# Kernel tuning notes

Measured on AMD Instinct MI355X. Metric: run time of the kernel, lower is better.

## Reference

```python
import jax, jax.numpy as jnp
import numpy as np

B, L, E, H, D = 2, 2048, 2048, 16, 128
EPS = 1e-6


def _rms(x, scale):
    # RMSNorm over head_dim, computed in float32 (matches torch RMSNorm)
    x32 = x.astype(jnp.float32)
    n = jnp.mean(x32 * x32, axis=-1, keepdims=True)
    return (scale.astype(jnp.float32) * (x32 * jax.lax.rsqrt(n + EPS))).astype(x.dtype)


def _rotary(x, rope):
    # x: [B, L, H, D]; rope: [B, L, D//2, 2]
    xs = x.astype(jnp.float32).reshape(*x.shape[:-1], -1, 2)  # [B,L,H,D/2,2]
    rc = rope.reshape(xs.shape[0], xs.shape[1], 1, xs.shape[3], 2).astype(jnp.float32)
    out = jnp.stack(
        [xs[..., 0] * rc[..., 0] - xs[..., 1] * rc[..., 1],
         xs[..., 1] * rc[..., 0] + xs[..., 0] * rc[..., 1]], -1)
    return out.reshape(x.shape).astype(x.dtype)


def setup_inputs() -> dict:
    key = jax.random.key(0)
    ks = jax.random.split(key, 9)
    s = 0.02  # weight init scale (~kaiming fan_in for E=2048)
    return {
        "inputs_q": jax.random.normal(ks[0], (B, L, E), jnp.float32),
        "inputs_kv": jax.random.normal(ks[1], (B, L, E), jnp.float32),
        "bias": jax.random.normal(ks[2], (B, 1, L, L), jnp.float32),
        "rope_q": jax.random.normal(ks[3], (B, L, D // 2, 2), jnp.float32),
        "rope_k": jax.random.normal(ks[4], (B, L, D // 2, 2), jnp.float32),
        "Wq": jax.random.normal(ks[5], (E, E), jnp.float32) * s,
        "Wk": jax.random.normal(ks[6], (E, E), jnp.float32) * s,
        "Wv": jax.random.normal(ks[7], (E, E), jnp.float32) * s,
        "Wo": jax.random.normal(ks[8], (E, E), jnp.float32) * s,
        "q_scale": jnp.ones((D,), jnp.float32),
        "k_scale": jnp.ones((D,), jnp.float32),
    }


def reference(inputs_q, inputs_kv, bias, rope_q, rope_k, Wq, Wk, Wv, Wo, q_scale, k_scale):
    Bq, Lq, _ = inputs_q.shape
    Lk = inputs_kv.shape[1]
    dtype = inputs_q.dtype
    # QKV projections (torch Linear: y = x @ W.T)
    q = (inputs_q @ Wq.T).reshape(Bq, Lq, H, D)
    k = (inputs_kv @ Wk.T).reshape(Bq, Lk, H, D)
    v = (inputs_kv @ Wv.T).reshape(Bq, Lk, H, D)
    # qk_norm
    q = _rms(q, q_scale)
    k = _rms(k, k_scale)
    # rotary embeddings
    q = _rotary(q, rope_q)
    k = _rotary(k, rope_k)
    # float32_logits
    q = q.astype(jnp.float32)
    k = k.astype(jnp.float32)
    # faithful to torch source: query.div_(depth ** (-0.5)) == q * sqrt(D)
    q = q / (D ** (-0.5))
    logits = jnp.einsum('bqhd,bkhd->bhqk', q, k) + bias.astype(jnp.float32)
    probs = jax.nn.softmax(logits, axis=-1).astype(dtype)
    # dropout_rate = 0.0 -> identity
    x = jnp.einsum('bhqk,bkhd->bqhd', probs, v).reshape(Bq, Lq, E)
    return x @ Wo.T
```

## Files before the change

### kernel.cpp

```cpp
#include <hip/hip_runtime.h>

#define Bb 2
#define Ll 2048
#define Ee 2048
#define Hh 16
#define Dd 128
#define BL (Bb * Ll)
#define NT (Ll / 64)
#define LOSCALE 1024.0f
#define INV_LOSCALE (1.0f / 1024.0f)

typedef float f32x4 __attribute__((ext_vector_type(4)));
typedef _Float16 f16x8 __attribute__((ext_vector_type(8)));

__device__ __forceinline__ void gld_lds16(const void* g, void* l) {
  __builtin_amdgcn_global_load_lds((const __attribute__((address_space(1))) void*)g,
                                   (__attribute__((address_space(3))) void*)l, 16, 0, 0);
}

__global__ __launch_bounds__(256) void cvt_f32_f16(const float* __restrict__ in,
                                                   _Float16* __restrict__ out, int n4) {
  int i = blockIdx.x * 256 + threadIdx.x;
  if (i < n4) {
    float4 f = ((const float4*)in)[i];
    _Float16 o[4] = {(_Float16)f.x, (_Float16)f.y, (_Float16)f.z, (_Float16)f.w};
    ((uint2*)out)[i] = *(uint2*)o;
  }
}

__global__ __launch_bounds__(256) void cvt_split(const float* __restrict__ in,
                                                 _Float16* __restrict__ hi,
                                                 _Float16* __restrict__ lo, int n4) {
  int i = blockIdx.x * 256 + threadIdx.x;
  if (i < n4) {
    float4 f = ((const float4*)in)[i];
    float fa[4] = {f.x, f.y, f.z, f.w};
    _Float16 h[4], l[4];
    for (int j = 0; j < 4; ++j) {
      h[j] = (_Float16)fa[j];
      l[j] = (_Float16)((fa[j] - (float)h[j]) * LOSCALE);
    }
    ((uint2*)hi)[i] = *(uint2*)h;
    ((uint2*)lo)[i] = *(uint2*)l;
  }
}

__global__ __launch_bounds__(256) void bias_perm(const float* __restrict__ bias,
                                                 _Float16* __restrict__ out) {
  __shared__ float T[128][68];
  const int kt = blockIdx.x, qt = blockIdx.y, b = blockIdx.z;
  const float* src = bias + ((size_t)b * Ll + qt * 128) * Ll + kt * 64;
  const int t = threadIdx.x;
  for (int c = 0; c < 8; ++c) {
    int idx = c * 256 + t;
    int r = idx >> 4, col4 = (idx & 15) * 4;
    float4 v = *(const float4*)&src[(size_t)r * Ll + col4];
    T[r][col4 + 0] = v.x; T[r][col4 + 1] = v.y;
    T[r][col4 + 2] = v.z; T[r][col4 + 3] = v.w;
  }
  __syncthreads();
  _Float16* dst = out + (((size_t)(b * 16 + qt) * NT + kt) * 8) * 64 * 16;
  for (int s = 0; s < 2; ++s) {
    int slot = t + s * 256;
    int w = slot >> 6, lane = slot & 63;
    int quad = lane >> 4, l16 = lane & 15;
    _Float16 vals[16];
    for (int nt = 0; nt < 4; ++nt)
      for (int r = 0; r < 4; ++r)
        vals[nt * 4 + r] = (_Float16)T[w * 16 + quad * 4 + r][nt * 16 + l16];
    *(uint4*)&dst[(size_t)slot * 16] = *(uint4*)&vals[0];
    *(uint4*)&dst[(size_t)slot * 16 + 8] = *(uint4*)&vals[8];
  }
}

template <typename OutT>
__global__ __launch_bounds__(256, 2) void gemm_bt(const _Float16* __restrict__ A,
                                                  const _Float16* __restrict__ Bw,
                                                  OutT* __restrict__ C, int M, int N, int K) {
  __shared__ _Float16 As[128 * 64];
  __shared__ _Float16 Bs[128 * 64];
  const int tid = threadIdx.x;
  const int wave = tid >> 6, lane = tid & 63;
  const int quad = lane >> 4, l16 = lane & 15;
  const int lrow = lane >> 3, lch = lane & 7;
  const int scol = (lch ^ lrow) * 8;
  const int bm = blockIdx.y * 128, bn = blockIdx.x * 128;
  const int wm = (wave >> 1) * 64, wn = (wave & 1) * 64;

  f32x4 acc[4][4] = {};

  for (int k0 = 0; k0 < K; k0 += 64) {
    for (int i = 0; i < 4; ++i) {
      int br = wave * 32 + i * 8;
      gld_lds16(&A[(size_t)(bm + br + lrow) * K + k0 + scol], &As[br * 64]);
      gld_lds16(&Bw[(size_t)(bn + br + lrow) * K + k0 + scol], &Bs[br * 64]);
    }
    __syncthreads();
    for (int ks = 0; ks < 2; ++ks) {
      f16x8 af[4], bf[4];
      for (int mt = 0; mt < 4; ++mt)
        af[mt] = *(const f16x8*)&As[(wm + mt * 16 + l16) * 64 +
                                    (((ks * 4 + quad) ^ (l16 & 7)) * 8)];
      for (int nt = 0; nt < 4; ++nt)
        bf[nt] = *(const f16x8*)&Bs[(wn + nt * 16 + l16) * 64 +
                                    (((ks * 4 + quad) ^ (l16 & 7)) * 8)];
      for (int mt = 0; mt < 4; ++mt)
        for (int nt = 0; nt < 4; ++nt)
          acc[mt][nt] = __builtin_amdgcn_mfma_f32_16x16x32_f16(af[mt], bf[nt], acc[mt][nt], 0, 0, 0);
    }
    __syncthreads();
  }

  for (int mt = 0; mt < 4; ++mt)
    for (int nt = 0; nt < 4; ++nt)
      for (int r = 0; r < 4; ++r) {
        int m = bm + wm + mt * 16 + quad * 4 + r;
        int n = bn + wn + nt * 16 + l16;
        C[(size_t)m * N + n] = (OutT)acc[mt][nt][r];
      }
}

__global__ __launch_bounds__(256, 2) void gemm_bt_split(
    const _Float16* __restrict__ Ah, const _Float16* __restrict__ Al,
    const _Float16* __restrict__ Bh, const _Float16* __restrict__ Bl,
    float* __restrict__ C, int M, int N, int K) {
  __shared__ _Float16 Ash[128 * 64];
  __shared__ _Float16 Asl[128 * 64];
  __shared__ _Float16 Bsh[128 * 64];
  __shared__ _Float16 Bsl[128 * 64];
  const int tid = threadIdx.x;
  const int wave = tid >> 6, lane = tid & 63;
  const int quad = lane >> 4, l16 = lane & 15;
  const int lrow = lane >> 3, lch = lane & 7;
  const int scol = (lch ^ lrow) * 8;
  const int bm = blockIdx.y * 128, bn = blockIdx.x * 128;
  const int wm = (wave >> 1) * 64, wn = (wave & 1) * 64;

  f32x4 acc_hh[4][4] = {};
  f32x4 acc_cr[4][4] = {};

  for (int k0 = 0; k0 < K; k0 += 64) {
    for (int i = 0; i < 4; ++i) {
      int br = wave * 32 + i * 8;
      size_t ga = (size_t)(bm + br + lrow) * K + k0 + scol;
      size_t gb = (size_t)(bn + br + lrow) * K + k0 + scol;
      gld_lds16(&Ah[ga], &Ash[br * 64]);
      gld_lds16(&Al[ga], &Asl[br * 64]);
      gld_lds16(&Bh[gb], &Bsh[br * 64]);
      gld_lds16(&Bl[gb], &Bsl[br * 64]);
    }
    __syncthreads();
    for (int ks = 0; ks < 2; ++ks) {
      const int sw = ((ks * 4 + quad) ^ (l16 & 7)) * 8;
      f16x8 afh[4], afl[4], bfh[4], bfl[4];
      for (int mt = 0; mt < 4; ++mt) {
        afh[mt] = *(const f16x8*)&Ash[(wm + mt * 16 + l16) * 64 + sw];
        afl[mt] = *(const f16x8*)&Asl[(wm + mt * 16 + l16) * 64 + sw];
      }
      for (int nt = 0; nt < 4; ++nt) {
        bfh[nt] = *(const f16x8*)&Bsh[(wn + nt * 16 + l16) * 64 + sw];
        bfl[nt] = *(const f16x8*)&Bsl[(wn + nt * 16 + l16) * 64 + sw];
      }
      for (int mt = 0; mt < 4; ++mt)
        for (int nt = 0; nt < 4; ++nt) {
          acc_hh[mt][nt] = __builtin_amdgcn_mfma_f32_16x16x32_f16(afh[mt], bfh[nt], acc_hh[mt][nt], 0, 0, 0);
          acc_cr[mt][nt] = __builtin_amdgcn_mfma_f32_16x16x32_f16(afh[mt], bfl[nt], acc_cr[mt][nt], 0, 0, 0);
          acc_cr[mt][nt] = __builtin_amdgcn_mfma_f32_16x16x32_f16(afl[mt], bfh[nt], acc_cr[mt][nt], 0, 0, 0);
        }
    }
    __syncthreads();
  }

  for (int mt = 0; mt < 4; ++mt)
    for (int nt = 0; nt < 4; ++nt)
      for (int r = 0; r < 4; ++r) {
        int m = bm + wm + mt * 16 + quad * 4 + r;
        int n = bn + wn + nt * 16 + l16;
        C[(size_t)m * N + n] = acc_hh[mt][nt][r] + acc_cr[mt][nt][r] * INV_LOSCALE;
      }
}

__global__ __launch_bounds__(256) void transpose_v(const _Float16* __restrict__ V,
                                                   _Float16* __restrict__ Vt) {
  __shared__ _Float16 T[64][72];
  const int bl0 = blockIdx.x * 64, n0 = blockIdx.y * 64;
  const int tid = threadIdx.x;
  for (int c = 0; c < 2; ++c) {
    int chunk = tid + c * 256;
    int r = chunk >> 3, cc = (chunk & 7) * 8;
    *(uint4*)&T[r][cc] = *(const uint4*)&V[(size_t)(bl0 + r) * Ee + n0 + cc];
  }
  __syncthreads();
  const int b = bl0 >> 11;
  const int k0 = bl0 & (Ll - 1);
  for (int c = 0; c < 2; ++c) {
    int chunk = tid + c * 256;
    int nr = chunk >> 3, kc = (chunk & 7) * 8;
    _Float16 tmp[8];
    for (int j = 0; j < 8; ++j) tmp[j] = T[kc + j][nr];
    *(uint4*)&Vt[((size_t)b * Ee + n0 + nr) * Ll + k0 + kc] = *(uint4*)tmp;
  }
}

__global__ __launch_bounds__(256) void rmsrope(const float* __restrict__ raw,
                                               const float* __restrict__ scale,
                                               const float* __restrict__ rope,
                                               _Float16* __restrict__ outh,
                                               _Float16* __restrict__ outl, float outmul) {
  int row = blockIdx.x * 4 + (threadIdx.x >> 6);
  int t = threadIdx.x & 63;
  float2 x = *(const float2*)&raw[(size_t)row * Dd + 2 * t];
  float ss = x.x * x.x + x.y * x.y;
  for (int off = 1; off < 64; off <<= 1) ss += __shfl_xor(ss, off);
  float inv = rsqrtf(ss * (1.0f / Dd) + 1e-6f);
  float2 sc = *(const float2*)&scale[2 * t];
  float y0 = x.x * inv * sc.x;
  float y1 = x.y * inv * sc.y;
  int bl = row >> 4;
  float2 cs = *(const float2*)&rope[(size_t)bl * Dd + 2 * t];
  float r0 = (y0 * cs.x - y1 * cs.y) * outmul;
  float r1 = (y1 * cs.x + y0 * cs.y) * outmul;
  _Float16 h[2] = {(_Float16)r0, (_Float16)r1};
  _Float16 l[2] = {(_Float16)((r0 - (float)h[0]) * LOSCALE),
                   (_Float16)((r1 - (float)h[1]) * LOSCALE)};
  *(uint*)&outh[(size_t)row * Dd + 2 * t] = *(uint*)h;
  *(uint*)&outl[(size_t)row * Dd + 2 * t] = *(uint*)l;
}

__global__ __launch_bounds__(512, 2) void attn(const _Float16* __restrict__ Qh_,
                                               const _Float16* __restrict__ Ql_,
                                               const _Float16* __restrict__ Kh_,
                                               const _Float16* __restrict__ Kl_,
                                               const _Float16* __restrict__ Vt_g,
                                               const _Float16* __restrict__ biasp,
                                               _Float16* __restrict__ O) {
  __shared__ _Float16 Ksh[2][64 * 128];
  __shared__ _Float16 Ksl[2][64 * 128];
  __shared__ _Float16 Vts[2][128 * 64];
  __shared__ _Float16 Ps[128 * 72];

  const int tid = threadIdx.x;
  const int wave = tid >> 6, lane = tid & 63;
  const int quad = lane >> 4, l16 = lane & 15;
  const int lrow8 = lane >> 3, lch8 = lane & 7;
  const int lrow16 = lane >> 4, lch16 = lane & 15;
  const int h = blockIdx.x;
  const int qt = blockIdx.y, q0 = qt * 128;
  const int b = blockIdx.z;

  f16x8 aqh[4], aql[4];
  {
    size_t qrow = (((size_t)b * Ll + q0 + wave * 16 + l16) * Hh + h) * Dd;
    for (int ks = 0; ks < 4; ++ks) {
      aqh[ks] = *(const f16x8*)&Qh_[qrow + ks * 32 + quad * 8];
      aql[ks] = *(const f16x8*)&Ql_[qrow + ks * 32 + quad * 8];
    }
  }
  const _Float16* Vbase = Vt_g + ((size_t)b * Ee + h * Dd) * Ll;
  const _Float16* bias_w =
      biasp + (((size_t)(b * 16 + qt) * NT * 8 + wave) * 64 + lane) * 16;

  f32x4 o_acc[8] = {};
  float m_r[4], l_r[4];
  for (int r = 0; r < 4; ++r) { m_r[r] = -1e30f; l_r[r] = 0.f; }

  auto stage = [&](int nb, int kt) {
    const int k0 = kt * 64;
    for (int i = 0; i < 2; ++i) {
      int br = wave * 8 + i * 4;
      int row = br + lrow16;
      int sc = (lch16 ^ (row & 7)) * 8;
      size_t g = (((size_t)b * Ll + k0 + row) * Hh + h) * Dd + sc;
      gld_lds16(&Kh_[g], &Ksh[nb][br * 128]);
      gld_lds16(&Kl_[g], &Ksl[nb][br * 128]);
    }
    for (int i = 0; i < 2; ++i) {
      int br = wave * 16 + i * 8;
      int row = br + lrow8;
      int sc = (lch8 ^ (row & 7)) * 8;
      gld_lds16(&Vbase[(size_t)row * Ll + k0 + sc], &Vts[nb][br * 64]);
    }
  };

  stage(0, 0);
  __syncthreads();

  for (int kt = 0; kt < NT; ++kt) {
    const int cur = kt & 1;
    if (kt + 1 < NT) stage(cur ^ 1, kt + 1);

    f16x8 bf0 = *(const f16x8*)&bias_w[(size_t)kt * 8192];
    f16x8 bf1 = *(const f16x8*)&bias_w[(size_t)kt * 8192 + 8];

    f32x4 s_hh[4] = {}, s_cr[4] = {};
    for (int ks = 0; ks < 4; ++ks) {
      const int sw = ((ks * 4 + quad) ^ (l16 & 7)) * 8;
      for (int nt = 0; nt < 4; ++nt) {
        f16x8 bkh = *(const f16x8*)&Ksh[cur][(nt * 16 + l16) * 128 + sw];
        f16x8 bkl = *(const f16x8*)&Ksl[cur][(nt * 16 + l16) * 128 + sw];
        s_hh[nt] = __builtin_amdgcn_mfma_f32_16x16x32_f16(aqh[ks], bkh, s_hh[nt], 0, 0, 0);
        s_cr[nt] = __builtin_amdgcn_mfma_f32_16x16x32_f16(aqh[ks], bkl, s_cr[nt], 0, 0, 0);
        s_cr[nt] = __builtin_amdgcn_mfma_f32_16x16x32_f16(aql[ks], bkh, s_cr[nt], 0, 0, 0);
      }
    }
#pragma unroll
    for (int nt = 0; nt < 4; ++nt)
#pragma unroll
      for (int r = 0; r < 4; ++r) {
        float bv = (nt < 2) ? (float)bf0[nt * 4 + r] : (float)bf1[nt * 4 + r - 8];
        s_hh[nt][r] += s_cr[nt][r] * INV_LOSCALE + bv;
      }

    float alpha[4];
    for (int r = 0; r < 4; ++r) {
      float x = fmaxf(fmaxf(s_hh[0][r], s_hh[1][r]), fmaxf(s_hh[2][r], s_hh[3][r]));
      for (int off = 1; off < 16; off <<= 1) x = fmaxf(x, __shfl_xor(x, off));
      float mn = fmaxf(m_r[r], x);
      alpha[r] = __expf(m_r[r] - mn);
      m_r[r] = mn;
    }
    for (int r = 0; r < 4; ++r) {
      float sum = 0.f;
      for (int nt = 0; nt < 4; ++nt) {
        float p = __expf(s_hh[nt][r] - m_r[r]);
        sum += p;
        Ps[(wave * 16 + quad * 4 + r) * 72 + nt * 16 + l16] = (_Float16)p;
      }
      for (int off = 1; off < 16; off <<= 1) sum += __shfl_xor(sum, off);
      l_r[r] = l_r[r] * alpha[r] + sum;
    }
    for (int ot = 0; ot < 8; ++ot)
      for (int r = 0; r < 4; ++r) o_acc[ot][r] *= alpha[r];

    for (int ks = 0; ks < 2; ++ks) {
      const int sw = ((ks * 4 + quad) ^ (l16 & 7)) * 8;
      f16x8 ap = *(const f16x8*)&Ps[(wave * 16 + l16) * 72 + ks * 32 + quad * 8];
      for (int ot = 0; ot < 8; ++ot) {
        f16x8 bv = *(const f16x8*)&Vts[cur][(ot * 16 + l16) * 64 + sw];
        o_acc[ot] = __builtin_amdgcn_mfma_f32_16x16x32_f16(ap, bv, o_acc[ot], 0, 0, 0);
      }
    }
    __syncthreads();
  }

  for (int ot = 0; ot < 8; ++ot)
    for (int r = 0; r < 4; ++r) {
      int m = q0 + wave * 16 + quad * 4 + r;
      O[(((size_t)b * Ll + m) * Hh + h) * Dd + ot * 16 + l16] =
          (_Float16)(o_acc[ot][r] / l_r[r]);
    }
}

extern "C" void kernel_launch(void* const* d_in, const int* in_sizes, int n_in,
                              void* d_out, int out_size, void* d_ws, size_t ws_size,
                              hipStream_t stream) {
  const float* inputs_q  = (const float*)d_in[0];
  const float* inputs_kv = (const float*)d_in[1];
  const float* bias      = (const float*)d_in[2];
  const float* rope_q    = (const float*)d_in[3];
  const float* rope_k    = (const float*)d_in[4];
  const float* Wq        = (const float*)d_in[5];
  const float* Wk        = (const float*)d_in[6];
  const float* Wv        = (const float*)d_in[7];
  const float* Wo        = (const float*)d_in[8];
  const float* q_scale   = (const float*)d_in[9];
  const float* k_scale   = (const float*)d_in[10];
  float* out = (float*)d_out;

  char* ws = (char*)d_ws;
  size_t o = 0;
  auto alloc = [&](size_t bytes) {
    char* p = ws + o;
    o += (bytes + 255) & ~(size_t)255;
    return p;
  };
  const size_t szX16 = (size_t)BL * Ee * 2;
  const size_t szW16 = (size_t)Ee * Ee * 2;
  _Float16* Xq_hi  = (_Float16*)alloc(szX16);
  _Float16* Xq_lo  = (_Float16*)alloc(szX16);
  _Float16* Xkv_hi = (_Float16*)alloc(szX16);
  _Float16* Xkv_lo = (_Float16*)alloc(szX16);
  _Float16* Wq_hi  = (_Float16*)alloc(szW16);
  _Float16* Wq_lo  = (_Float16*)alloc(szW16);
  _Float16* Wk_hi  = (_Float16*)alloc(szW16);
  _Float16* Wk_lo  = (_Float16*)alloc(szW16);
  _Float16* Wv_hi  = (_Float16*)alloc(szW16);
  _Float16* Wo_hi  = (_Float16*)alloc(szW16);
  float* Qraw = (float*)alloc((size_t)BL * Ee * 4);
  float* Kraw = (float*)alloc((size_t)BL * Ee * 4);
  _Float16* V16 = (_Float16*)alloc(szX16);
  _Float16* Q16h   = Xq_hi;
  _Float16* Q16l   = Xq_lo;
  _Float16* K16h   = Xkv_hi;
  _Float16* K16l   = Xkv_lo;
  _Float16* X16    = (_Float16*)Qraw;
  _Float16* Vt_g   = Wq_hi;
  _Float16* biasp  = (_Float16*)Kraw;

  const int nX4 = BL * Ee / 4;
  const int nW4 = Ee * Ee / 4;
  cvt_split<<<nX4 / 256, 256, 0, stream>>>(inputs_q, Xq_hi, Xq_lo, nX4);
  cvt_split<<<nX4 / 256, 256, 0, stream>>>(inputs_kv, Xkv_hi, Xkv_lo, nX4);
  cvt_split<<<nW4 / 256, 256, 0, stream>>>(Wq, Wq_hi, Wq_lo, nW4);
  cvt_split<<<nW4 / 256, 256, 0, stream>>>(Wk, Wk_hi, Wk_lo, nW4);
  cvt_f32_f16<<<nW4 / 256, 256, 0, stream>>>(Wv, Wv_hi, nW4);
  cvt_f32_f16<<<nW4 / 256, 256, 0, stream>>>(Wo, Wo_hi, nW4);

  dim3 gblk(Ee / 128, BL / 128);
  gemm_bt_split<<<gblk, 256, 0, stream>>>(Xq_hi, Xq_lo, Wq_hi, Wq_lo, Qraw, BL, Ee, Ee);
  gemm_bt_split<<<gblk, 256, 0, stream>>>(Xkv_hi, Xkv_lo, Wk_hi, Wk_lo, Kraw, BL, Ee, Ee);
  gemm_bt<_Float16><<<gblk, 256, 0, stream>>>(Xkv_hi, Wv_hi, V16, BL, Ee, Ee);

  transpose_v<<<dim3(BL / 64, Ee / 64), 256, 0, stream>>>(V16, Vt_g);

  rmsrope<<<BL * Hh / 4, 256, 0, stream>>>(Qraw, q_scale, rope_q, Q16h, Q16l, sqrtf((float)Dd));
  rmsrope<<<BL * Hh / 4, 256, 0, stream>>>(Kraw, k_scale, rope_k, K16h, K16l, 1.0f);

  bias_perm<<<dim3(NT, Ll / 128, Bb), 256, 0, stream>>>(bias, biasp);

  attn<<<dim3(Hh, Ll / 128, Bb), 512, 0, stream>>>(Q16h, Q16l, K16h, K16l, Vt_g, biasp, X16);

  gemm_bt<float><<<gblk, 256, 0, stream>>>(X16, Wo_hi, out, BL, Ee, Ee);
}
```

Baseline: 744.7 us.

## Double attention query tile per block, use exp2 softmax with lazy rescaling

The attention kernel now processes 256 query rows per block, with each wave handling two 16-row tiles. This halves K/V staging traffic per query and reuses each K/V LDS fragment across two MFMAs. The log2e factor is folded into the Q scaling and the bias so that softmax can use exp2. The running-max rescale is skipped unless the max grows by more than 8, and the row-sum shuffle reduction is deferred to the epilogue. The lo-part LOSCALE is removed so all three split MFMAs accumulate into one accumulator, and setprio hints plus an XOR-swizzled P buffer are added. The cost is doubled accumulator register pressure, and the unscaled fp16 lo parts may lose precision to subnormals.

```diff
diff --git a/kernel.cpp b/kernel.cpp
--- a/kernel.cpp
+++ b/kernel.cpp
@@ -9,6 +9,7 @@
 #define NT (Ll / 64)
 #define LOSCALE 1024.0f
 #define INV_LOSCALE (1.0f / 1024.0f)
+#define LOG2E 1.442695041f
 
 typedef float f32x4 __attribute__((ext_vector_type(4)));
 typedef _Float16 f16x8 __attribute__((ext_vector_type(8)));
@@ -59,7 +60,7 @@
     T[r][col4 + 2] = v.z; T[r][col4 + 3] = v.w;
   }
   __syncthreads();
-  _Float16* dst = out + (((size_t)(b * 16 + qt) * NT + kt) * 8) * 64 * 16;
+  _Float16* dst = out + ((((size_t)(b * 8 + (qt >> 1)) * NT + kt) * 16 + (qt & 1) * 8) * 64) * 16;
   for (int s = 0; s < 2; ++s) {
     int slot = t + s * 256;
     int w = slot >> 6, lane = slot & 63;
@@ -67,9 +68,9 @@
     _Float16 vals[16];
     for (int nt = 0; nt < 4; ++nt)
       for (int r = 0; r < 4; ++r)
-        vals[nt * 4 + r] = (_Float16)T[w * 16 + quad * 4 + r][nt * 16 + l16];
-    *(uint4*)&dst[(size_t)slot * 16] = *(uint4*)&vals[0];
-    *(uint4*)&dst[(size_t)slot * 16 + 8] = *(uint4*)&vals[8];
+        vals[nt * 4 + r] = (_Float16)(T[w * 16 + quad * 4 + r][nt * 16 + l16] * LOG2E);
+    *(uint4*)&dst[((size_t)w * 64 + lane) * 16] = *(uint4*)&vals[0];
+    *(uint4*)&dst[((size_t)w * 64 + lane) * 16 + 8] = *(uint4*)&vals[8];
   }
 }
 
@@ -221,8 +222,7 @@
   float r0 = (y0 * cs.x - y1 * cs.y) * outmul;
   float r1 = (y1 * cs.x + y0 * cs.y) * outmul;
   _Float16 h[2] = {(_Float16)r0, (_Float16)r1};
-  _Float16 l[2] = {(_Float16)((r0 - (float)h[0]) * LOSCALE),
-                   (_Float16)((r1 - (float)h[1]) * LOSCALE)};
+  _Float16 l[2] = {(_Float16)(r0 - (float)h[0]), (_Float16)(r1 - (float)h[1])};
   *(uint*)&outh[(size_t)row * Dd + 2 * t] = *(uint*)h;
   *(uint*)&outl[(size_t)row * Dd + 2 * t] = *(uint*)l;
 }
@@ -237,7 +237,7 @@
   __shared__ _Float16 Ksh[2][64 * 128];
   __shared__ _Float16 Ksl[2][64 * 128];
   __shared__ _Float16 Vts[2][128 * 64];
-  __shared__ _Float16 Ps[128 * 72];
+  __shared__ _Float16 Ps[256 * 64];
 
   const int tid = threadIdx.x;
   const int wave = tid >> 6, lane = tid & 63;
@@ -245,24 +245,25 @@
   const int lrow8 = lane >> 3, lch8 = lane & 7;
   const int lrow16 = lane >> 4, lch16 = lane & 15;
   const int h = blockIdx.x;
-  const int qt = blockIdx.y, q0 = qt * 128;
+  const int qt = blockIdx.y, q0 = qt * 256;
   const int b = blockIdx.z;
 
-  f16x8 aqh[4], aql[4];
-  {
-    size_t qrow = (((size_t)b * Ll + q0 + wave * 16 + l16) * Hh + h) * Dd;
+  f16x8 aqh[2][4], aql[2][4];
+  for (int m = 0; m < 2; ++m) {
+    size_t qrow = (((size_t)b * Ll + q0 + wave * 32 + m * 16 + l16) * Hh + h) * Dd;
     for (int ks = 0; ks < 4; ++ks) {
-      aqh[ks] = *(const f16x8*)&Qh_[qrow + ks * 32 + quad * 8];
-      aql[ks] = *(const f16x8*)&Ql_[qrow + ks * 32 + quad * 8];
+      aqh[m][ks] = *(const f16x8*)&Qh_[qrow + ks * 32 + quad * 8];
+      aql[m][ks] = *(const f16x8*)&Ql_[qrow + ks * 32 + quad * 8];
     }
   }
   const _Float16* Vbase = Vt_g + ((size_t)b * Ee + h * Dd) * Ll;
-  const _Float16* bias_w =
-      biasp + (((size_t)(b * 16 + qt) * NT * 8 + wave) * 64 + lane) * 16;
-
-  f32x4 o_acc[8] = {};
-  float m_r[4], l_r[4];
-  for (int r = 0; r < 4; ++r) { m_r[r] = -1e30f; l_r[r] = 0.f; }
+  const _Float16* bias_base = biasp + (size_t)(b * 8 + qt) * NT * 16 * 1024 +
+                              (size_t)(wave * 2) * 1024 + (size_t)lane * 16;
+
+  f32x4 o_acc[2][8] = {};
+  float m_r[2][4], l_r[2][4];
+  for (int m = 0; m < 2; ++m)
+    for (int r = 0; r < 4; ++r) { m_r[m][r] = -1e30f; l_r[m][r] = 0.f; }
 
   auto stage = [&](int nb, int kt) {
     const int k0 = kt * 64;
@@ -287,68 +288,106 @@
 
   for (int kt = 0; kt < NT; ++kt) {
     const int cur = kt & 1;
+
+    f16x8 bf[2][2];
+    for (int m = 0; m < 2; ++m) {
+      const _Float16* bp = bias_base + ((size_t)kt * 16 + m) * 1024;
+      bf[m][0] = *(const f16x8*)&bp[0];
+      bf[m][1] = *(const f16x8*)&bp[8];
+    }
     if (kt + 1 < NT) stage(cur ^ 1, kt + 1);
 
-    f16x8 bf0 = *(const f16x8*)&bias_w[(size_t)kt * 8192];
-    f16x8 bf1 = *(const f16x8*)&bias_w[(size_t)kt * 8192 + 8];
-
-    f32x4 s_hh[4] = {}, s_cr[4] = {};
+    __builtin_amdgcn_s_setprio(1);
+    f32x4 s[2][4] = {};
     for (int ks = 0; ks < 4; ++ks) {
       const int sw = ((ks * 4 + quad) ^ (l16 & 7)) * 8;
       for (int nt = 0; nt < 4; ++nt) {
         f16x8 bkh = *(const f16x8*)&Ksh[cur][(nt * 16 + l16) * 128 + sw];
         f16x8 bkl = *(const f16x8*)&Ksl[cur][(nt * 16 + l16) * 128 + sw];
-        s_hh[nt] = __builtin_amdgcn_mfma_f32_16x16x32_f16(aqh[ks], bkh, s_hh[nt], 0, 0, 0);
-        s_cr[nt] = __builtin_amdgcn_mfma_f32_16x16x32_f16(aqh[ks], bkl, s_cr[nt], 0, 0, 0);
-        s_cr[nt] = __builtin_amdgcn_mfma_f32_16x16x32_f16(aql[ks], bkh, s_cr[nt], 0, 0, 0);
-      }
-    }
+        for (int m = 0; m < 2; ++m) {
+          s[m][nt] = __builtin_amdgcn_mfma_f32_16x16x32_f16(aqh[m][ks], bkh, s[m][nt], 0, 0, 0);
+          s[m][nt] = __builtin_amdgcn_mfma_f32_16x16x32_f16(aql[m][ks], bkh, s[m][nt], 0, 0, 0);
+          s[m][nt] = __builtin_amdgcn_mfma_f32_16x16x32_f16(aqh[m][ks], bkl, s[m][nt], 0, 0, 0);
+        }
+      }
+    }
+    __builtin_amdgcn_s_setprio(0);
+
 #pragma unroll
-    for (int nt = 0; nt < 4; ++nt)
+    for (int m = 0; m < 2; ++m)
 #pragma unroll
+      for (int nt = 0; nt < 4; ++nt)
+#pragma unroll
+        for (int r = 0; r < 4; ++r) {
+          float bv = (nt < 2) ? (float)bf[m][0][nt * 4 + r] : (float)bf[m][1][nt * 4 + r - 8];
+          s[m][nt][r] += bv;
+        }
+
+    float x[2][4];
+    bool grow = false;
+    for (int m = 0; m < 2; ++m)
       for (int r = 0; r < 4; ++r) {
-        float bv = (nt < 2) ? (float)bf0[nt * 4 + r] : (float)bf1[nt * 4 + r - 8];
-        s_hh[nt][r] += s_cr[nt][r] * INV_LOSCALE + bv;
-      }
-
-    float alpha[4];
-    for (int r = 0; r < 4; ++r) {
-      float x = fmaxf(fmaxf(s_hh[0][r], s_hh[1][r]), fmaxf(s_hh[2][r], s_hh[3][r]));
-      for (int off = 1; off < 16; off <<= 1) x = fmaxf(x, __shfl_xor(x, off));
-      float mn = fmaxf(m_r[r], x);
-      alpha[r] = __expf(m_r[r] - mn);
-      m_r[r] = mn;
-    }
-    for (int r = 0; r < 4; ++r) {
-      float sum = 0.f;
-      for (int nt = 0; nt < 4; ++nt) {
-        float p = __expf(s_hh[nt][r] - m_r[r]);
-        sum += p;
-        Ps[(wave * 16 + quad * 4 + r) * 72 + nt * 16 + l16] = (_Float16)p;
-      }
-      for (int off = 1; off < 16; off <<= 1) sum += __shfl_xor(sum, off);
-      l_r[r] = l_r[r] * alpha[r] + sum;
-    }
-    for (int ot = 0; ot < 8; ++ot)
-      for (int r = 0; r < 4; ++r) o_acc[ot][r] *= alpha[r];
-
+        float v = fmaxf(fmaxf(s[m][0][r], s[m][1][r]), fmaxf(s[m][2][r], s[m][3][r]));
+        for (int off = 1; off < 16; off <<= 1) v = fmaxf(v, __shfl_xor(v, off));
+        x[m][r] = v;
+        grow |= (v > m_r[m][r] + 8.f);
+      }
+    if (__any(grow)) {
+      for (int m = 0; m < 2; ++m)
+        for (int r = 0; r < 4; ++r) {
+          float mn = fmaxf(m_r[m][r], x[m][r]);
+          float alpha = exp2f(m_r[m][r] - mn);
+          m_r[m][r] = mn;
+          l_r[m][r] *= alpha;
+          for (int ot = 0; ot < 8; ++ot) o_acc[m][ot][r] *= alpha;
+        }
+    }
+    for (int m = 0; m < 2; ++m)
+      for (int r = 0; r < 4; ++r) {
+        int row = wave * 32 + m * 16 + quad * 4 + r;
+        float sum = 0.f;
+        for (int nt = 0; nt < 4; ++nt) {
+          float p = exp2f(s[m][nt][r] - m_r[m][r]);
+          sum += p;
+          int col = nt * 16 + l16;
+          Ps[row * 64 + (col ^ (((row >> 2) & 3) << 4))] = (_Float16)p;
+        }
+        l_r[m][r] += sum;
+      }
+
+    __builtin_amdgcn_s_setprio(1);
     for (int ks = 0; ks < 2; ++ks) {
       const int sw = ((ks * 4 + quad) ^ (l16 & 7)) * 8;
-      f16x8 ap = *(const f16x8*)&Ps[(wave * 16 + l16) * 72 + ks * 32 + quad * 8];
+      f16x8 ap[2];
+      for (int m = 0; m < 2; ++m) {
+        int prow = wave * 32 + m * 16 + l16;
+        ap[m] = *(const f16x8*)&Ps[prow * 64 +
+                                   ((ks * 32 + quad * 8) ^ (((l16 >> 2) & 3) << 4))];
+      }
       for (int ot = 0; ot < 8; ++ot) {
         f16x8 bv = *(const f16x8*)&Vts[cur][(ot * 16 + l16) * 64 + sw];
-        o_acc[ot] = __builtin_amdgcn_mfma_f32_16x16x32_f16(ap, bv, o_acc[ot], 0, 0, 0);
-      }
-    }
+        for (int m = 0; m < 2; ++m)
+          o_acc[m][ot] = __builtin_amdgcn_mfma_f32_16x16x32_f16(ap[m], bv, o_acc[m][ot], 0, 0, 0);
+      }
+    }
+    __builtin_amdgcn_s_setprio(0);
     __syncthreads();
   }
 
-  for (int ot = 0; ot < 8; ++ot)
+  for (int m = 0; m < 2; ++m)
     for (int r = 0; r < 4; ++r) {
-      int m = q0 + wave * 16 + quad * 4 + r;
-      O[(((size_t)b * Ll + m) * Hh + h) * Dd + ot * 16 + l16] =
-          (_Float16)(o_acc[ot][r] / l_r[r]);
-    }
+      float l = l_r[m][r];
+      for (int off = 1; off < 16; off <<= 1) l += __shfl_xor(l, off);
+      l_r[m][r] = 1.f / l;
+    }
+
+  for (int m = 0; m < 2; ++m)
+    for (int ot = 0; ot < 8; ++ot)
+      for (int r = 0; r < 4; ++r) {
+        int mm = q0 + wave * 32 + m * 16 + quad * 4 + r;
+        O[(((size_t)b * Ll + mm) * Hh + h) * Dd + ot * 16 + l16] =
+            (_Float16)(o_acc[m][ot][r] * l_r[m][r]);
+      }
 }
 
 extern "C" void kernel_launch(void* const* d_in, const int* in_sizes, int n_in,
@@ -413,12 +452,13 @@
 
   transpose_v<<<dim3(BL / 64, Ee / 64), 256, 0, stream>>>(V16, Vt_g);
 
-  rmsrope<<<BL * Hh / 4, 256, 0, stream>>>(Qraw, q_scale, rope_q, Q16h, Q16l, sqrtf((float)Dd));
+  rmsrope<<<BL * Hh / 4, 256, 0, stream>>>(Qraw, q_scale, rope_q, Q16h, Q16l,
+                                           sqrtf((float)Dd) * LOG2E);
   rmsrope<<<BL * Hh / 4, 256, 0, stream>>>(Kraw, k_scale, rope_k, K16h, K16l, 1.0f);
 
   bias_perm<<<dim3(NT, Ll / 128, Bb), 256, 0, stream>>>(bias, biasp);
 
-  attn<<<dim3(Hh, Ll / 128, Bb), 512, 0, stream>>>(Q16h, Q16l, K16h, K16l, Vt_g, biasp, X16);
+  attn<<<dim3(Hh, Ll / 256, Bb), 512, 0, stream>>>(Q16h, Q16l, K16h, K16l, Vt_g, biasp, X16);
 
   gemm_bt<float><<<gblk, 256, 0, stream>>>(X16, Wo_hi, out, BL, Ee, Ee);
 }
```

Measured after the change: 735.6 us. Within noise of the previous version (-1.2%).

## Rework attention softmax with exp2, lazy rescale, single K buffer and swizzled P

Applied to the files above, without the earlier changes.

Folds log2(e) into Q scaling and bias so softmax uses the hardware exp2 directly, and skips the online-softmax rescale unless a row max grows past a threshold. The row-sum reduction moves to the end, and the lo-part correction is accumulated into one accumulator without the LOSCALE scaling. K is single-buffered and P uses an XOR-swizzled layout without padding to cut LDS and allow more occupancy (launch bounds raised to 4). MFMA sections get raised priority. The risks are fp16 precision loss from an unscaled lo residual and the loss of K prefetch overlap.

```diff
diff --git a/kernel.cpp b/kernel.cpp
--- a/kernel.cpp
+++ b/kernel.cpp
@@ -9,6 +9,7 @@
 #define NT (Ll / 64)
 #define LOSCALE 1024.0f
 #define INV_LOSCALE (1.0f / 1024.0f)
+#define LOG2E 1.442695041f
 
 typedef float f32x4 __attribute__((ext_vector_type(4)));
 typedef _Float16 f16x8 __attribute__((ext_vector_type(8)));
@@ -16,6 +17,12 @@
 __device__ __forceinline__ void gld_lds16(const void* g, void* l) {
   __builtin_amdgcn_global_load_lds((const __attribute__((address_space(1))) void*)g,
                                    (__attribute__((address_space(3))) void*)l, 16, 0, 0);
+}
+
+__device__ __forceinline__ float exp2_hw(float x) {
+  float r;
+  asm("v_exp_f32 %0, %1" : "=v"(r) : "v"(x));
+  return r;
 }
 
 __global__ __launch_bounds__(256) void cvt_f32_f16(const float* __restrict__ in,
@@ -59,7 +66,7 @@
     T[r][col4 + 2] = v.z; T[r][col4 + 3] = v.w;
   }
   __syncthreads();
-  _Float16* dst = out + (((size_t)(b * 16 + qt) * NT + kt) * 8) * 64 * 16;
+  _Float16* dst = out + ((((size_t)(b * 8 + (qt >> 1)) * NT + kt) * 16 + (qt & 1) * 8) * 64) * 16;
   for (int s = 0; s < 2; ++s) {
     int slot = t + s * 256;
     int w = slot >> 6, lane = slot & 63;
@@ -67,9 +74,9 @@
     _Float16 vals[16];
     for (int nt = 0; nt < 4; ++nt)
       for (int r = 0; r < 4; ++r)
-        vals[nt * 4 + r] = (_Float16)T[w * 16 + quad * 4 + r][nt * 16 + l16];
-    *(uint4*)&dst[(size_t)slot * 16] = *(uint4*)&vals[0];
-    *(uint4*)&dst[(size_t)slot * 16 + 8] = *(uint4*)&vals[8];
+        vals[nt * 4 + r] = (_Float16)(T[w * 16 + quad * 4 + r][nt * 16 + l16] * LOG2E);
+    *(uint4*)&dst[((size_t)w * 64 + lane) * 16] = *(uint4*)&vals[0];
+    *(uint4*)&dst[((size_t)w * 64 + lane) * 16 + 8] = *(uint4*)&vals[8];
   }
 }
 
@@ -221,23 +228,22 @@
   float r0 = (y0 * cs.x - y1 * cs.y) * outmul;
   float r1 = (y1 * cs.x + y0 * cs.y) * outmul;
   _Float16 h[2] = {(_Float16)r0, (_Float16)r1};
-  _Float16 l[2] = {(_Float16)((r0 - (float)h[0]) * LOSCALE),
-                   (_Float16)((r1 - (float)h[1]) * LOSCALE)};
+  _Float16 l[2] = {(_Float16)(r0 - (float)h[0]), (_Float16)(r1 - (float)h[1])};
   *(uint*)&outh[(size_t)row * Dd + 2 * t] = *(uint*)h;
   *(uint*)&outl[(size_t)row * Dd + 2 * t] = *(uint*)l;
 }
 
-__global__ __launch_bounds__(512, 2) void attn(const _Float16* __restrict__ Qh_,
+__global__ __launch_bounds__(512, 4) void attn(const _Float16* __restrict__ Qh_,
                                                const _Float16* __restrict__ Ql_,
                                                const _Float16* __restrict__ Kh_,
                                                const _Float16* __restrict__ Kl_,
                                                const _Float16* __restrict__ Vt_g,
                                                const _Float16* __restrict__ biasp,
                                                _Float16* __restrict__ O) {
-  __shared__ _Float16 Ksh[2][64 * 128];
-  __shared__ _Float16 Ksl[2][64 * 128];
+  __shared__ _Float16 Ksh[64 * 128];
+  __shared__ _Float16 Ksl[64 * 128];
   __shared__ _Float16 Vts[2][128 * 64];
-  __shared__ _Float16 Ps[128 * 72];
+  __shared__ _Float16 Ps[128 * 64];
 
   const int tid = threadIdx.x;
   const int wave = tid >> 6, lane = tid & 63;
@@ -257,23 +263,26 @@
     }
   }
   const _Float16* Vbase = Vt_g + ((size_t)b * Ee + h * Dd) * Ll;
-  const _Float16* bias_w =
-      biasp + (((size_t)(b * 16 + qt) * NT * 8 + wave) * 64 + lane) * 16;
+  const _Float16* bias_base = biasp + (size_t)(b * 8 + (qt >> 1)) * (NT * 16 * 1024) +
+                              (size_t)((qt & 1) * 8 + wave) * 1024 + (size_t)lane * 16;
 
   f32x4 o_acc[8] = {};
   float m_r[4], l_r[4];
   for (int r = 0; r < 4; ++r) { m_r[r] = -1e30f; l_r[r] = 0.f; }
 
-  auto stage = [&](int nb, int kt) {
+  auto stageK = [&](int kt) {
     const int k0 = kt * 64;
     for (int i = 0; i < 2; ++i) {
       int br = wave * 8 + i * 4;
       int row = br + lrow16;
       int sc = (lch16 ^ (row & 7)) * 8;
       size_t g = (((size_t)b * Ll + k0 + row) * Hh + h) * Dd + sc;
-      gld_lds16(&Kh_[g], &Ksh[nb][br * 128]);
-      gld_lds16(&Kl_[g], &Ksl[nb][br * 128]);
-    }
+      gld_lds16(&Kh_[g], &Ksh[br * 128]);
+      gld_lds16(&Kl_[g], &Ksl[br * 128]);
+    }
+  };
+  auto stageV = [&](int nb, int kt) {
+    const int k0 = kt * 64;
     for (int i = 0; i < 2; ++i) {
       int br = wave * 16 + i * 8;
       int row = br + lrow8;
@@ -282,72 +291,104 @@
     }
   };
 
-  stage(0, 0);
+  stageK(0);
+  stageV(0, 0);
   __syncthreads();
 
   for (int kt = 0; kt < NT; ++kt) {
     const int cur = kt & 1;
-    if (kt + 1 < NT) stage(cur ^ 1, kt + 1);
-
-    f16x8 bf0 = *(const f16x8*)&bias_w[(size_t)kt * 8192];
-    f16x8 bf1 = *(const f16x8*)&bias_w[(size_t)kt * 8192 + 8];
-
-    f32x4 s_hh[4] = {}, s_cr[4] = {};
+
+    f16x8 bf0 = *(const f16x8*)&bias_base[(size_t)kt * 16384];
+    f16x8 bf1 = *(const f16x8*)&bias_base[(size_t)kt * 16384 + 8];
+
+    __builtin_amdgcn_s_setprio(1);
+    f32x4 s[4] = {};
     for (int ks = 0; ks < 4; ++ks) {
       const int sw = ((ks * 4 + quad) ^ (l16 & 7)) * 8;
       for (int nt = 0; nt < 4; ++nt) {
-        f16x8 bkh = *(const f16x8*)&Ksh[cur][(nt * 16 + l16) * 128 + sw];
-        f16x8 bkl = *(const f16x8*)&Ksl[cur][(nt * 16 + l16) * 128 + sw];
-        s_hh[nt] = __builtin_amdgcn_mfma_f32_16x16x32_f16(aqh[ks], bkh, s_hh[nt], 0, 0, 0);
-        s_cr[nt] = __builtin_amdgcn_mfma_f32_16x16x32_f16(aqh[ks], bkl, s_cr[nt], 0, 0, 0);
-        s_cr[nt] = __builtin_amdgcn_mfma_f32_16x16x32_f16(aql[ks], bkh, s_cr[nt], 0, 0, 0);
-      }
-    }
+        f16x8 bkh = *(const f16x8*)&Ksh[(nt * 16 + l16) * 128 + sw];
+        f16x8 bkl = *(const f16x8*)&Ksl[(nt * 16 + l16) * 128 + sw];
+        s[nt] = __builtin_amdgcn_mfma_f32_16x16x32_f16(aqh[ks], bkh, s[nt], 0, 0, 0);
+        s[nt] = __builtin_amdgcn_mfma_f32_16x16x32_f16(aql[ks], bkh, s[nt], 0, 0, 0);
+        s[nt] = __builtin_amdgcn_mfma_f32_16x16x32_f16(aqh[ks], bkl, s[nt], 0, 0, 0);
+      }
+    }
+    __builtin_amdgcn_s_setprio(0);
+
+    __syncthreads();
+
+    if (kt + 1 < NT) {
+      stageK(kt + 1);
+      stageV(cur ^ 1, kt + 1);
+    }
+
 #pragma unroll
     for (int nt = 0; nt < 4; ++nt)
 #pragma unroll
       for (int r = 0; r < 4; ++r) {
         float bv = (nt < 2) ? (float)bf0[nt * 4 + r] : (float)bf1[nt * 4 + r - 8];
-        s_hh[nt][r] += s_cr[nt][r] * INV_LOSCALE + bv;
-      }
-
-    float alpha[4];
+        s[nt][r] += bv;
+      }
+
+    bool grow = false;
+#pragma unroll
     for (int r = 0; r < 4; ++r) {
-      float x = fmaxf(fmaxf(s_hh[0][r], s_hh[1][r]), fmaxf(s_hh[2][r], s_hh[3][r]));
-      for (int off = 1; off < 16; off <<= 1) x = fmaxf(x, __shfl_xor(x, off));
-      float mn = fmaxf(m_r[r], x);
-      alpha[r] = __expf(m_r[r] - mn);
-      m_r[r] = mn;
-    }
+      float v = fmaxf(fmaxf(s[0][r], s[1][r]), fmaxf(s[2][r], s[3][r]));
+      grow = grow || (v > m_r[r] + 8.f);
+    }
+    if (__any(grow)) {
+#pragma unroll
+      for (int r = 0; r < 4; ++r) {
+        float v = fmaxf(fmaxf(s[0][r], s[1][r]), fmaxf(s[2][r], s[3][r]));
+        for (int off = 1; off < 16; off <<= 1) v = fmaxf(v, __shfl_xor(v, off));
+        float mn = fmaxf(m_r[r], v);
+        float alpha = exp2_hw(m_r[r] - mn);
+        m_r[r] = mn;
+        l_r[r] *= alpha;
+        for (int ot = 0; ot < 8; ++ot) o_acc[ot][r] *= alpha;
+      }
+    }
+#pragma unroll
     for (int r = 0; r < 4; ++r) {
+      int row = wave * 16 + quad * 4 + r;
       float sum = 0.f;
+#pragma unroll
       for (int nt = 0; nt < 4; ++nt) {
-        float p = __expf(s_hh[nt][r] - m_r[r]);
+        float p = exp2_hw(s[nt][r] - m_r[r]);
         sum += p;
-        Ps[(wave * 16 + quad * 4 + r) * 72 + nt * 16 + l16] = (_Float16)p;
-      }
-      for (int off = 1; off < 16; off <<= 1) sum += __shfl_xor(sum, off);
-      l_r[r] = l_r[r] * alpha[r] + sum;
-    }
-    for (int ot = 0; ot < 8; ++ot)
-      for (int r = 0; r < 4; ++r) o_acc[ot][r] *= alpha[r];
-
+        int col = nt * 16 + l16;
+        Ps[row * 64 + (col ^ (((row >> 2) & 3) << 4))] = (_Float16)p;
+      }
+      l_r[r] += sum;
+    }
+
+    __builtin_amdgcn_s_setprio(1);
     for (int ks = 0; ks < 2; ++ks) {
       const int sw = ((ks * 4 + quad) ^ (l16 & 7)) * 8;
-      f16x8 ap = *(const f16x8*)&Ps[(wave * 16 + l16) * 72 + ks * 32 + quad * 8];
+      int prow = wave * 16 + l16;
+      f16x8 ap = *(const f16x8*)&Ps[prow * 64 +
+                                    ((ks * 32 + quad * 8) ^ (((l16 >> 2) & 3) << 4))];
       for (int ot = 0; ot < 8; ++ot) {
         f16x8 bv = *(const f16x8*)&Vts[cur][(ot * 16 + l16) * 64 + sw];
         o_acc[ot] = __builtin_amdgcn_mfma_f32_16x16x32_f16(ap, bv, o_acc[ot], 0, 0, 0);
       }
     }
-    __syncthreads();
+    __builtin_amdgcn_s_setprio(0);
+
+    __syncthreads();
+  }
+
+  for (int r = 0; r < 4; ++r) {
+    float l = l_r[r];
+    for (int off = 1; off < 16; off <<= 1) l += __shfl_xor(l, off);
+    l_r[r] = 1.f / l;
   }
 
   for (int ot = 0; ot < 8; ++ot)
     for (int r = 0; r < 4; ++r) {
-      int m = q0 + wave * 16 + quad * 4 + r;
-      O[(((size_t)b * Ll + m) * Hh + h) * Dd + ot * 16 + l16] =
-          (_Float16)(o_acc[ot][r] / l_r[r]);
+      int mm = q0 + wave * 16 + quad * 4 + r;
+      O[(((size_t)b * Ll + mm) * Hh + h) * Dd + ot * 16 + l16] =
+          (_Float16)(o_acc[ot][r] * l_r[r]);
     }
 }
 
@@ -413,7 +454,8 @@
 
   transpose_v<<<dim3(BL / 64, Ee / 64), 256, 0, stream>>>(V16, Vt_g);
 
-  rmsrope<<<BL * Hh / 4, 256, 0, stream>>>(Qraw, q_scale, rope_q, Q16h, Q16l, sqrtf((float)Dd));
+  rmsrope<<<BL * Hh / 4, 256, 0, stream>>>(Qraw, q_scale, rope_q, Q16h, Q16l,
+                                           sqrtf((float)Dd) * LOG2E);
   rmsrope<<<BL * Hh / 4, 256, 0, stream>>>(Kraw, k_scale, rope_k, K16h, K16l, 1.0f);
 
   bias_perm<<<dim3(NT, Ll / 128, Bb), 256, 0, stream>>>(bias, biasp);
```

New measurement: 825.9 us. +10.9%, slower.
